# Optimization experiments

Measured on AMD Instinct MI355X. Metric: run time of the kernel, lower is better.

The kernel has to match this reference:

```python
import math
import jax, jax.numpy as jnp
import numpy as np

NH = 16          # num attention heads
NOPE = 128       # qk_nope_head_dim
ROPE = 64        # qk_rope_head_dim
VD = 128         # v_head_dim
QLR = 1536       # q_lora_rank
IH = 8           # index_n_heads
ID = 128         # index_head_dim
TOPK = 8         # index_topk
EPS = 1e-5


def layernorm(x, w, b):
    mu = jnp.mean(x, axis=-1, keepdims=True)
    var = jnp.mean((x - mu) ** 2, axis=-1, keepdims=True)
    return (x - mu) * jax.lax.rsqrt(var + EPS) * w + b


def rope_tables(dim, end, base=10000.0):
    freqs = 1.0 / (base ** (jnp.arange(0, dim, 2, dtype=jnp.float32) / dim))  # [dim//2]
    t = jnp.arange(end, dtype=jnp.float32)
    f = jnp.outer(t, freqs)  # [end, dim//2]
    return jnp.cos(f), jnp.sin(f)


def apply_rope(x, cos, sin):
    # x: [b, h, s, d]; cos/sin: [s, d//2] (interleaved real/imag pairs)
    xr, xi = x[..., 0::2], x[..., 1::2]
    c = cos[None, None, :, :]
    s = sin[None, None, :, :]
    or_, oi = xr * c - xi * s, xr * s + xi * c
    return jnp.stack([or_, oi], axis=-1).reshape(x.shape)


def setup_inputs() -> dict:
    key = jax.random.key(0)
    ks = jax.random.split(key, 16)
    H = 2048
    B, S = 2, 2048
    w = lambda k, shp: (jax.random.normal(k, shp, dtype=jnp.float32) * 0.02)
    return {
        "x": jax.random.normal(ks[0], (B, S, H), dtype=jnp.float32),
        "W_cq": w(ks[1], (H, QLR)),
        "q_norm_w": jnp.ones((QLR,), jnp.float32),
        "q_norm_b": jnp.zeros((QLR,), jnp.float32),
        "W_q": w(ks[2], (QLR, NH * (NOPE + ROPE))),
        "W_ckv": w(ks[3], (H, NH * (NOPE + ROPE))),
        "kv_norm_w": jnp.ones((NOPE,), jnp.float32),
        "kv_norm_b": jnp.zeros((NOPE,), jnp.float32),
        "W_kv": w(ks[4], (NOPE, NOPE + VD)),
        "W_o": w(ks[5], (NH * VD, H)),
        "W_ip": w(ks[6], (H, IH * ID)),
        "W_ig": w(ks[7], (H, IH)),
        "W_sq": w(ks[8], (ID, ID)),
        "W_sk": w(ks[9], (ID, ID)),
        "W_sv": w(ks[10], (ID, ID)),
        "W_io": w(ks[11], (ID, H)),
    }


def _forward(x, W_cq, q_norm_w, q_norm_b, W_q, W_ckv, kv_norm_w, kv_norm_b,
             W_kv, W_o, W_ip, W_ig, W_sq, W_sk, W_sv, W_io):
    B, S, H = x.shape
    # --- MLA dense path ---
    qc = layernorm(x @ W_cq, q_norm_w, q_norm_b)                  # [B,S,QLR]
    qp = (qc @ W_q).reshape(B, S, NH, NOPE + ROPE).transpose(0, 2, 1, 3)
    q_nope, q_pe = qp[..., :NOPE], qp[..., NOPE:]
    kvc = (x @ W_ckv).reshape(B, S, NH, ROPE + NOPE).transpose(0, 2, 1, 3)
    k_pe, kv_nope = kvc[..., :ROPE], kvc[..., ROPE:]
    kv_n = layernorm(kv_nope, kv_norm_w, kv_norm_b)               # [B,NH,S,NOPE]
    kvp = kv_n @ W_kv                                             # [B,NH,S,NOPE+VD]
    k_nope, v = kvp[..., :NOPE], kvp[..., NOPE:]
    cos, sin = rope_tables(ROPE, S)
    q_pe = apply_rope(q_pe, cos, sin)
    k_pe = apply_rope(k_pe, cos, sin)
    q = jnp.concatenate([q_nope, q_pe], axis=-1)                  # [B,NH,S,192]
    k = jnp.concatenate([k_nope, k_pe], axis=-1)
    scale = 1.0 / math.sqrt(NOPE + ROPE)
    scores = jnp.einsum("bhqd,bhkd->bhqk", q, k) * scale
    causal = jnp.triu(jnp.ones((S, S), dtype=bool), k=1)
    scores = jnp.where(causal[None, None], -jnp.inf, scores)
    probs = jax.nn.softmax(scores.astype(jnp.float32), axis=-1).astype(q.dtype)
    attn = jnp.einsum("bhqk,bhkd->bhqd", probs, v)                # [B,NH,S,VD]
    # --- NSA sparse path (lightning indexer) ---
    ist = (x @ W_ip).reshape(B, S, IH, ID).transpose(0, 2, 1, 3)  # [B,IH,S,ID]
    gate = (x @ W_ig).transpose(0, 2, 1)                          # [B,IH,S]
    _, top_idx = jax.lax.top_k(gate, TOPK)                        # [B,IH,TOPK]
    sel = jnp.take_along_axis(ist, top_idx[..., None], axis=2)    # [B,IH,TOPK,ID]
    sq, sk, sv = sel @ W_sq, sel @ W_sk, sel @ W_sv
    ss = jnp.einsum("bhqd,bhkd->bhqk", sq, sk) / math.sqrt(ID)    # [B,IH,TOPK,TOPK]
    sp = jax.nn.softmax(ss.astype(jnp.float32), axis=-1).astype(sq.dtype)
    so = jnp.einsum("bhqk,bhkd->bhqd", sp, sv)                    # [B,IH,TOPK,ID]
    sparse_out = so @ W_io                                        # [B,IH,TOPK,H]
    io = sparse_out.mean(axis=2)[:, :, None, :VD]                 # [B,IH,1,VD]
    io = jnp.broadcast_to(io, (B, IH, S, VD))
    io = jnp.repeat(io, NH // IH, axis=1)                         # [B,NH,S,VD]
    attn = attn + io
    out = attn.transpose(0, 2, 1, 3).reshape(B, S, NH * VD) @ W_o
    return out


def reference(x, W_cq, q_norm_w, q_norm_b, W_q, W_ckv, kv_norm_w, kv_norm_b,
              W_kv, W_o, W_ip, W_ig, W_sq, W_sk, W_sv, W_io):
    return _forward(x, W_cq, q_norm_w, q_norm_b, W_q, W_ckv, kv_norm_w,
                    kv_norm_b, W_kv, W_o, W_ip, W_ig, W_sq, W_sk, W_sv, W_io)
```

## Files before the change

### kernel.cpp

```cpp
#include <hip/hip_runtime.h>
#include <hip/hip_bf16.h>
#include <math.h>

#define NH    16
#define NOPE  128
#define ROPED 64
#define VD    128
#define QLR   1536
#define IH    8
#define ID    128
#define TOPK  8
#define EPSF  1e-5f
#define B_    2
#define S_    2048
#define H_    2048

using bf16 = __hip_bfloat16;
typedef __attribute__((ext_vector_type(8))) short short8;
typedef __attribute__((ext_vector_type(4))) short short4v;
typedef __attribute__((ext_vector_type(4))) float f32x4;

#define GLOBAL_AS __attribute__((address_space(1)))
#define LDS_AS    __attribute__((address_space(3)))

__device__ __forceinline__ float b2f(bf16 v) { return __bfloat162float(v); }
__device__ __forceinline__ bf16 f2b(float v) { return __float2bfloat16(v); }
__device__ __forceinline__ void stoC(float* p, float v) { *p = v; }
__device__ __forceinline__ void stoC(bf16* p, float v) { *p = __float2bfloat16(v); }

__global__ __launch_bounds__(256) void gate_k(const float* __restrict__ x,
                                              const float* __restrict__ Wg,
                                              float* __restrict__ gate) {
    const int t = threadIdx.x;
    const int wid = t >> 6, lane = t & 63;
    const int row = blockIdx.x * 4 + wid;
    const float* xp = x + (size_t)row * H_;

    float acc[8] = {};
    for (int k0 = 0; k0 < H_; k0 += 256) {
        const int kb = k0 + lane * 4;
        const f32x4 xv = *(const f32x4*)(xp + kb);
        const f32x4 w0 = *(const f32x4*)(Wg + (size_t)kb * 8);
        const f32x4 w1 = *(const f32x4*)(Wg + (size_t)kb * 8 + 4);
        const f32x4 w2 = *(const f32x4*)(Wg + (size_t)(kb + 1) * 8);
        const f32x4 w3 = *(const f32x4*)(Wg + (size_t)(kb + 1) * 8 + 4);
        const f32x4 w4 = *(const f32x4*)(Wg + (size_t)(kb + 2) * 8);
        const f32x4 w5 = *(const f32x4*)(Wg + (size_t)(kb + 2) * 8 + 4);
        const f32x4 w6 = *(const f32x4*)(Wg + (size_t)(kb + 3) * 8);
        const f32x4 w7 = *(const f32x4*)(Wg + (size_t)(kb + 3) * 8 + 4);
#pragma unroll
        for (int j = 0; j < 4; j++) {
            acc[j]     += xv[0] * w0[j] + xv[1] * w2[j] + xv[2] * w4[j] + xv[3] * w6[j];
            acc[4 + j] += xv[0] * w1[j] + xv[1] * w3[j] + xv[2] * w5[j] + xv[3] * w7[j];
        }
    }
#pragma unroll
    for (int j = 0; j < 8; j++) {
#pragma unroll
        for (int off = 32; off > 0; off >>= 1)
            acc[j] += __shfl_xor(acc[j], off);
    }
    if (lane == 0) {
#pragma unroll
        for (int j = 0; j < 8; j++) gate[(size_t)row * 8 + j] = acc[j];
    }
}

template <typename OT>
__global__ __launch_bounds__(256) void gemm_bt_mfma_k(const bf16* __restrict__ A,
                                                      const bf16* __restrict__ Bt,
                                                      OT* __restrict__ C,
                                                      int M, int N, int K) {
    __shared__ bf16 As[128 * 32];
    __shared__ bf16 Bs[128 * 32];
    const int t = threadIdx.x;
    const int w = t >> 6;
    const int l = t & 63;
    const int col = l & 15;
    const int quad = l >> 4;
    const int wm = w >> 1, wn = w & 1;

    const int gx = gridDim.x;
    const int nwg = gx * gridDim.y;
    const int lin = blockIdx.y * gx + blockIdx.x;
    const int work = (lin & 7) * (nwg >> 3) + (lin >> 3);
    const int row0 = (work / gx) * 128;
    const int col0 = (work % gx) * 128;

    const int rA = l >> 2;
    const int cA = (l & 3) * 8;
    const bf16* ga0 = A + (size_t)(row0 + w * 16 + rA) * K + cA;
    const bf16* ga1 = A + (size_t)(row0 + (4 + w) * 16 + rA) * K + cA;
    const bf16* gb0 = Bt + (size_t)(col0 + w * 16 + rA) * K + cA;
    const bf16* gb1 = Bt + (size_t)(col0 + (4 + w) * 16 + rA) * K + cA;
    bf16* lA0 = &As[w * 512];
    bf16* lA1 = &As[(4 + w) * 512];
    bf16* lB0 = &Bs[w * 512];
    bf16* lB1 = &Bs[(4 + w) * 512];

    f32x4 acc[4][4];
#pragma unroll
    for (int i = 0; i < 4; i++)
#pragma unroll
        for (int j = 0; j < 4; j++) acc[i][j] = (f32x4){0.f, 0.f, 0.f, 0.f};

    for (int k0 = 0; k0 < K; k0 += 32) {
        __syncthreads();
        __builtin_amdgcn_global_load_lds((const GLOBAL_AS void*)(ga0 + k0),
                                         (LDS_AS void*)lA0, 16, 0, 0);
        __builtin_amdgcn_global_load_lds((const GLOBAL_AS void*)(ga1 + k0),
                                         (LDS_AS void*)lA1, 16, 0, 0);
        __builtin_amdgcn_global_load_lds((const GLOBAL_AS void*)(gb0 + k0),
                                         (LDS_AS void*)lB0, 16, 0, 0);
        __builtin_amdgcn_global_load_lds((const GLOBAL_AS void*)(gb1 + k0),
                                         (LDS_AS void*)lB1, 16, 0, 0);
        __syncthreads();

        short8 af[4], bfr[4];
#pragma unroll
        for (int i = 0; i < 4; i++) {
            af[i]  = *(const short8*)&As[(wm * 64 + i * 16 + col) * 32 + quad * 8];
            bfr[i] = *(const short8*)&Bs[(wn * 64 + i * 16 + col) * 32 + quad * 8];
        }
#pragma unroll
        for (int i = 0; i < 4; i++)
#pragma unroll
            for (int j = 0; j < 4; j++)
                acc[i][j] = __builtin_amdgcn_mfma_f32_16x16x32_bf16(af[i], bfr[j], acc[i][j], 0, 0, 0);
    }

#pragma unroll
    for (int i = 0; i < 4; i++)
#pragma unroll
        for (int j = 0; j < 4; j++)
#pragma unroll
            for (int r = 0; r < 4; r++) {
                const int gr = row0 + wm * 64 + i * 16 + quad * 4 + r;
                const int gc = col0 + wn * 64 + j * 16 + col;
                stoC(C + (size_t)gr * N + gc, acc[i][j][r]);
            }
}

__global__ __launch_bounds__(256) void gemm_x3_k(const bf16* __restrict__ A,
                                                 const bf16* __restrict__ Bt,
                                                 float* __restrict__ cq,
                                                 bf16* __restrict__ kvc,
                                                 float* __restrict__ ist) {
    __shared__ bf16 As[128 * 32];
    __shared__ bf16 Bs[128 * 32];
    const int K = H_;
    const int t = threadIdx.x;
    const int w = t >> 6;
    const int l = t & 63;
    const int col = l & 15;
    const int quad = l >> 4;
    const int wm = w >> 1, wn = w & 1;

    const int gx = gridDim.x;
    const int nwg = gx * gridDim.y;
    const int lin = blockIdx.y * gx + blockIdx.x;
    const int work = (lin & 7) * (nwg >> 3) + (lin >> 3);
    const int row0 = (work / gx) * 128;
    const int col0 = (work % gx) * 128;

    const int rA = l >> 2;
    const int cA = (l & 3) * 8;
    const bf16* ga0 = A + (size_t)(row0 + w * 16 + rA) * K + cA;
    const bf16* ga1 = A + (size_t)(row0 + (4 + w) * 16 + rA) * K + cA;
    const bf16* gb0 = Bt + (size_t)(col0 + w * 16 + rA) * K + cA;
    const bf16* gb1 = Bt + (size_t)(col0 + (4 + w) * 16 + rA) * K + cA;
    bf16* lA0 = &As[w * 512];
    bf16* lA1 = &As[(4 + w) * 512];
    bf16* lB0 = &Bs[w * 512];
    bf16* lB1 = &Bs[(4 + w) * 512];

    f32x4 acc[4][4];
#pragma unroll
    for (int i = 0; i < 4; i++)
#pragma unroll
        for (int j = 0; j < 4; j++) acc[i][j] = (f32x4){0.f, 0.f, 0.f, 0.f};

    for (int k0 = 0; k0 < K; k0 += 32) {
        __syncthreads();
        __builtin_amdgcn_global_load_lds((const GLOBAL_AS void*)(ga0 + k0),
                                         (LDS_AS void*)lA0, 16, 0, 0);
        __builtin_amdgcn_global_load_lds((const GLOBAL_AS void*)(ga1 + k0),
                                         (LDS_AS void*)lA1, 16, 0, 0);
        __builtin_amdgcn_global_load_lds((const GLOBAL_AS void*)(gb0 + k0),
                                         (LDS_AS void*)lB0, 16, 0, 0);
        __builtin_amdgcn_global_load_lds((const GLOBAL_AS void*)(gb1 + k0),
                                         (LDS_AS void*)lB1, 16, 0, 0);
        __syncthreads();

        short8 af[4], bfr[4];
#pragma unroll
        for (int i = 0; i < 4; i++) {
            af[i]  = *(const short8*)&As[(wm * 64 + i * 16 + col) * 32 + quad * 8];
            bfr[i] = *(const short8*)&Bs[(wn * 64 + i * 16 + col) * 32 + quad * 8];
        }
#pragma unroll
        for (int i = 0; i < 4; i++)
#pragma unroll
            for (int j = 0; j < 4; j++)
                acc[i][j] = __builtin_amdgcn_mfma_f32_16x16x32_bf16(af[i], bfr[j], acc[i][j], 0, 0, 0);
    }

#pragma unroll
    for (int i = 0; i < 4; i++)
#pragma unroll
        for (int j = 0; j < 4; j++)
#pragma unroll
            for (int r = 0; r < 4; r++) {
                const int gr = row0 + wm * 64 + i * 16 + quad * 4 + r;
                const int gc = col0 + wn * 64 + j * 16 + col;
                const float v = acc[i][j][r];
                if (col0 < 1536)       cq[(size_t)gr * QLR + gc] = v;
                else if (col0 < 4608)  kvc[(size_t)gr * 3072 + (gc - 1536)] = f2b(v);
                else                   ist[(size_t)gr * 1024 + (gc - 4608)] = v;
            }
}

__global__ __launch_bounds__(256) void gemm_kv_k(const bf16* __restrict__ A,
                                                 const bf16* __restrict__ Bt,
                                                 bf16* __restrict__ kvc,
                                                 bf16* __restrict__ VbT) {
    __shared__ bf16 As[128 * 32];
    __shared__ bf16 Bs[128 * 32];
    const int K = 128;
    const int t = threadIdx.x;
    const int w = t >> 6;
    const int l = t & 63;
    const int col = l & 15;
    const int quad = l >> 4;
    const int wm = w >> 1, wn = w & 1;

    const int gx = gridDim.x;
    const int nwg = gx * gridDim.y;
    const int lin = blockIdx.y * gx + blockIdx.x;
    const int work = (lin & 7) * (nwg >> 3) + (lin >> 3);
    const int row0 = (work / gx) * 128;
    const int col0 = (work % gx) * 128;

    const int rA = l >> 2;
    const int cA = (l & 3) * 8;
    const bf16* ga0 = A + (size_t)(row0 + w * 16 + rA) * K + cA;
    const bf16* ga1 = A + (size_t)(row0 + (4 + w) * 16 + rA) * K + cA;
    const bf16* gb0 = Bt + (size_t)(col0 + w * 16 + rA) * K + cA;
    const bf16* gb1 = Bt + (size_t)(col0 + (4 + w) * 16 + rA) * K + cA;
    bf16* lA0 = &As[w * 512];
    bf16* lA1 = &As[(4 + w) * 512];
    bf16* lB0 = &Bs[w * 512];
    bf16* lB1 = &Bs[(4 + w) * 512];

    f32x4 acc[4][4];
#pragma unroll
    for (int i = 0; i < 4; i++)
#pragma unroll
        for (int j = 0; j < 4; j++) acc[i][j] = (f32x4){0.f, 0.f, 0.f, 0.f};

    for (int k0 = 0; k0 < K; k0 += 32) {
        __syncthreads();
        __builtin_amdgcn_global_load_lds((const GLOBAL_AS void*)(ga0 + k0),
                                         (LDS_AS void*)lA0, 16, 0, 0);
        __builtin_amdgcn_global_load_lds((const GLOBAL_AS void*)(ga1 + k0),
                                         (LDS_AS void*)lA1, 16, 0, 0);
        __builtin_amdgcn_global_load_lds((const GLOBAL_AS void*)(gb0 + k0),
                                         (LDS_AS void*)lB0, 16, 0, 0);
        __builtin_amdgcn_global_load_lds((const GLOBAL_AS void*)(gb1 + k0),
                                         (LDS_AS void*)lB1, 16, 0, 0);
        __syncthreads();

        short8 af[4], bfr[4];
#pragma unroll
        for (int i = 0; i < 4; i++) {
            af[i]  = *(const short8*)&As[(wm * 64 + i * 16 + col) * 32 + quad * 8];
            bfr[i] = *(const short8*)&Bs[(wn * 64 + i * 16 + col) * 32 + quad * 8];
        }
#pragma unroll
        for (int i = 0; i < 4; i++)
#pragma unroll
            for (int j = 0; j < 4; j++)
                acc[i][j] = __builtin_amdgcn_mfma_f32_16x16x32_bf16(af[i], bfr[j], acc[i][j], 0, 0, 0);
    }

    if (col0 == 0) {
#pragma unroll
        for (int i = 0; i < 4; i++)
#pragma unroll
            for (int j = 0; j < 4; j++)
#pragma unroll
                for (int r = 0; r < 4; r++) {
                    const int gr = row0 + wm * 64 + i * 16 + quad * 4 + r;
                    const int gc = wn * 64 + j * 16 + col;
                    kvc[(size_t)gr * 192 + gc] = f2b(acc[i][j][r]);
                }
    } else {
        const int bb = row0 >> 15;
        const int ssb = ((row0 >> 4) & (S_ - 1)) + wm * 4;
#pragma unroll
        for (int j = 0; j < 4; j++) {
            const int dv = wn * 64 + j * 16 + col;
#pragma unroll
            for (int r = 0; r < 4; r++) {
                const int hh = quad * 4 + r;
                short4v pk;
#pragma unroll
                for (int i = 0; i < 4; i++) {
                    bf16 v = f2b(acc[i][j][r]);
                    pk[i] = *(short*)&v;
                }
                *(short4v*)&VbT[((size_t)(bb * NH + hh) * 128 + dv) * S_ + ssb] = pk;
            }
        }
    }
}

__global__ __launch_bounds__(256) void kv_ln_k(bf16* __restrict__ kvc,
                                               const float* __restrict__ knw,
                                               const float* __restrict__ knb,
                                               bf16* __restrict__ kvn) {
    const int idx = blockIdx.x * 4 + (threadIdx.x >> 6);
    const int lane = threadIdx.x & 63;
    const int s = (idx >> 4) & (S_ - 1);
    const size_t base = (size_t)idx * 192;

    const float v0 = b2f(kvc[base + 64 + lane]);
    const float v1 = b2f(kvc[base + 128 + lane]);
    float xr = 0.f, xi = 0.f;
    if (lane < 32) { xr = b2f(kvc[base + 2 * lane]); xi = b2f(kvc[base + 2 * lane + 1]); }

    float s1 = v0 + v1, s2 = v0 * v0 + v1 * v1;
#pragma unroll
    for (int off = 32; off > 0; off >>= 1) {
        s1 += __shfl_xor(s1, off);
        s2 += __shfl_xor(s2, off);
    }
    const float mu = s1 * (1.f / 128.f);
    const float rinv = rsqrtf(s2 * (1.f / 128.f) - mu * mu + EPSF);
    kvn[(size_t)idx * 128 + lane]      = f2b((v0 - mu) * rinv * knw[lane] + knb[lane]);
    kvn[(size_t)idx * 128 + lane + 64] = f2b((v1 - mu) * rinv * knw[lane + 64] + knb[lane + 64]);

    if (lane < 32) {
        const float freq = exp2f(-0.41524101186092014f * (float)lane);
        const float ang = (float)s * freq;
        float sn, c; sincosf(ang, &sn, &c);
        kvc[base + 128 + 2 * lane]     = f2b(xr * c - xi * sn);
        kvc[base + 128 + 2 * lane + 1] = f2b(xr * sn + xi * c);
    }
}

__global__ __launch_bounds__(256) void cast_bf16_k(const float* __restrict__ X,
                                                   bf16* __restrict__ Y, int n4) {
    for (int i = blockIdx.x * 256 + threadIdx.x; i < n4; i += gridDim.x * 256) {
        const f32x4 v = ((const f32x4*)X)[i];
        short4v o;
#pragma unroll
        for (int j = 0; j < 4; j++) {
            bf16 b = f2b(v[j]);
            o[j] = *(short*)&b;
        }
        ((short4v*)Y)[i] = o;
    }
}

__global__ __launch_bounds__(256) void transpose_cast_k(const float* __restrict__ W,
                                                        bf16* __restrict__ Wt,
                                                        int K, int N) {
    __shared__ float tile[32][33];
    const int t = threadIdx.x;
    const int tx = t & 31, ty = t >> 5;
    const int n0 = blockIdx.x * 32;
    const int k0 = blockIdx.y * 32;
#pragma unroll
    for (int i = 0; i < 4; i++)
        tile[ty + 8 * i][tx] = W[(size_t)(k0 + ty + 8 * i) * N + n0 + tx];
    __syncthreads();
#pragma unroll
    for (int i = 0; i < 4; i++)
        Wt[(size_t)(n0 + ty + 8 * i) * K + k0 + tx] = f2b(tile[tx][ty + 8 * i]);
}

__global__ __launch_bounds__(256) void layernorm_cast_k(const float* __restrict__ X,
                                                        const float* __restrict__ w,
                                                        const float* __restrict__ b,
                                                        bf16* __restrict__ Y,
                                                        int L) {
    __shared__ float r1[256], r2[256];
    const int row = blockIdx.x;
    const int t = threadIdx.x;
    const float* xp = X + (size_t)row * L;
    bf16* yp = Y + (size_t)row * L;
    float s1 = 0.f, s2 = 0.f;
    for (int j = t; j < L; j += 256) { const float v = xp[j]; s1 += v; s2 += v * v; }
    r1[t] = s1; r2[t] = s2; __syncthreads();
    for (int off = 128; off > 0; off >>= 1) {
        if (t < off) { r1[t] += r1[t + off]; r2[t] += r2[t + off]; }
        __syncthreads();
    }
    const float mu   = r1[0] / (float)L;
    const float var  = r2[0] / (float)L - mu * mu;
    const float rinv = rsqrtf(var + EPSF);
    for (int j = t; j < L; j += 256)
        yp[j] = f2b((xp[j] - mu) * rinv * w[j] + b[j]);
}

__global__ __launch_bounds__(256) void q_rope_k(bf16* __restrict__ qp) {
    const int total = B_ * S_ * NH * 32;
    for (int p = blockIdx.x * 256 + threadIdx.x; p < total; p += gridDim.x * 256) {
        const int j = p & 31;
        const int row = p >> 5;
        const int sr = row >> 4;
        const int s = sr & (S_ - 1);
        const size_t base = (size_t)row * 192 + 128 + 2 * j;
        const float xr = b2f(qp[base]);
        const float xi = b2f(qp[base + 1]);
        const float freq = exp2f(-0.41524101186092014f * (float)j);
        const float ang = (float)s * freq;
        float sn, c; sincosf(ang, &sn, &c);
        qp[base]     = f2b(xr * c - xi * sn);
        qp[base + 1] = f2b(xr * sn + xi * c);
    }
}

__global__ __launch_bounds__(256) void sparse_k(const float* __restrict__ gate,
                                                const float* __restrict__ ist,
                                                const float* __restrict__ Wsq,
                                                const float* __restrict__ Wsk,
                                                const float* __restrict__ Wsv,
                                                const float* __restrict__ Wio,
                                                float* __restrict__ io) {
    __shared__ float g[S_];
    __shared__ float sel[TOPK][ID];
    __shared__ float sq[TOPK][ID], sk[TOPK][ID], sv[TOPK][ID];
    __shared__ float sp[TOPK][TOPK];
    __shared__ float ms[ID];
    __shared__ float rv[256];
    __shared__ int ri[256];
    __shared__ int sidx[TOPK];
    const int bi = blockIdx.x;
    const int ih = bi % IH;
    const int b = bi / IH;
    const int t = threadIdx.x;

    for (int s = t; s < S_; s += 256) g[s] = gate[(size_t)(b * S_ + s) * IH + ih];
    __syncthreads();

    for (int r = 0; r < TOPK; r++) {
        float bv = -INFINITY; int bx = S_;
        for (int s = t; s < S_; s += 256) {
            const float v = g[s];
            if (v > bv) { bv = v; bx = s; }
        }
        rv[t] = bv; ri[t] = bx; __syncthreads();
        for (int off = 128; off > 0; off >>= 1) {
            if (t < off) {
                const float v2 = rv[t + off]; const int i2 = ri[t + off];
                if (v2 > rv[t] || (v2 == rv[t] && i2 < ri[t])) { rv[t] = v2; ri[t] = i2; }
            }
            __syncthreads();
        }
        if (t == 0) { sidx[r] = ri[0]; g[ri[0]] = -INFINITY; }
        __syncthreads();
    }

    for (int i = t; i < TOPK * ID; i += 256) {
        const int r = i >> 7, d = i & 127;
        sel[r][d] = ist[((size_t)(b * S_ + sidx[r]) * IH + ih) * ID + d];
    }
    __syncthreads();

    for (int i = t; i < TOPK * ID; i += 256) {
        const int r = i >> 7, n = i & 127;
        float aq = 0.f, ak = 0.f, av = 0.f;
        for (int k = 0; k < 128; k++) {
            const float s = sel[r][k];
            aq += s * Wsq[k * ID + n];
            ak += s * Wsk[k * ID + n];
            av += s * Wsv[k * ID + n];
        }
        sq[r][n] = aq; sk[r][n] = ak; sv[r][n] = av;
    }
    __syncthreads();

    if (t < TOPK * TOPK) {
        const int r = t >> 3, c = t & 7;
        float a = 0.f;
        for (int k = 0; k < 128; k++) a += sq[r][k] * sk[c][k];
        sp[r][c] = a * 0.08838834764831845f;
    }
    __syncthreads();

    if (t < TOPK) {
        float m = -INFINITY;
        for (int c = 0; c < 8; c++) m = fmaxf(m, sp[t][c]);
        float e[8]; float sum = 0.f;
        for (int c = 0; c < 8; c++) { e[c] = expf(sp[t][c] - m); sum += e[c]; }
        for (int c = 0; c < 8; c++) sp[t][c] = e[c] / sum;
    }
    __syncthreads();

    if (t < ID) {
        float acc = 0.f;
        for (int r = 0; r < 8; r++) {
            float so = 0.f;
            for (int c = 0; c < 8; c++) so += sp[r][c] * sv[c][t];
            acc += so;
        }
        ms[t] = acc * 0.125f;
    }
    __syncthreads();

    if (t < ID) {
        float acc = 0.f;
        for (int k = 0; k < 128; k++) acc += ms[k] * Wio[(size_t)k * H_ + t];
        io[((size_t)b * IH + ih) * ID + t] = acc;
    }
}

__global__ __launch_bounds__(256, 2) void attn_mfma_k(const bf16* __restrict__ Qp,
                                                      const bf16* __restrict__ Kc,
                                                      const bf16* __restrict__ VbT,
                                                      const float* __restrict__ io,
                                                      bf16* __restrict__ O) {
    __shared__ unsigned short Kt[64 * 200];
    __shared__ unsigned short Vt[128 * 72];
    __shared__ unsigned short Ps[4 * 16 * 72];

    const int lin = blockIdx.x;
    const int qt = 31 - (lin >> 5);
    const int hb = lin & 31;
    const int h = hb & 15;
    const int b = hb >> 4;
    const int q0 = qt * 64;

    const int t = threadIdx.x;
    const int lane = t & 63;
    const int wq = t >> 6;
    const int col = lane & 15;
    const int quad = lane >> 4;

    const float scale = 0.07216878364870322f;
    const bf16* vplane = VbT + (size_t)(b * NH + h) * 128 * (size_t)S_;

    const int kr = t >> 2;
    const int kc0 = (t & 3) * 48;
    const int vki0 = (t & 7) * 8;
    const int vdv = t >> 3;

    short8 qfrag[6];
    {
        const int q = q0 + wq * 16 + col;
        const short8* qrow = (const short8*)(Qp + ((size_t)(b * S_ + q) * NH + h) * 192);
#pragma unroll
        for (int kc = 0; kc < 6; kc++) qfrag[kc] = qrow[kc * 4 + quad];
    }

    float m_r[4], l_r[4];
#pragma unroll
    for (int r = 0; r < 4; r++) { m_r[r] = -1e30f; l_r[r] = 0.f; }
    f32x4 accO[8];
#pragma unroll
    for (int nt = 0; nt < 8; nt++) accO[nt] = (f32x4){0.f, 0.f, 0.f, 0.f};

    const int nkt = qt + 1;

    short8 kreg[6], vreg[4];
    {
        const short8* ksrc = (const short8*)(Kc + ((size_t)(b * S_ + kr) * NH + h) * 192 + kc0);
#pragma unroll
        for (int c = 0; c < 6; c++) kreg[c] = ksrc[c];
#pragma unroll
        for (int p = 0; p < 4; p++)
            vreg[p] = *(const short8*)(vplane + (size_t)(p * 32 + vdv) * S_ + vki0);
    }

    for (int kt = 0; kt < nkt; kt++) {
        const int kt0 = kt * 64;
        __syncthreads();
        {
            short8* dst = (short8*)&Kt[kr * 200 + kc0];
#pragma unroll
            for (int c = 0; c < 6; c++) dst[c] = kreg[c];
#pragma unroll
            for (int p = 0; p < 4; p++)
                *(short8*)&Vt[(p * 32 + vdv) * 72 + vki0] = vreg[p];
        }
        __syncthreads();

        if (kt + 1 < nkt) {
            const int nk0 = kt0 + 64;
            const short8* ksrc = (const short8*)(Kc + ((size_t)(b * S_ + nk0 + kr) * NH + h) * 192 + kc0);
#pragma unroll
            for (int c = 0; c < 6; c++) kreg[c] = ksrc[c];
#pragma unroll
            for (int p = 0; p < 4; p++)
                vreg[p] = *(const short8*)(vplane + (size_t)(p * 32 + vdv) * S_ + nk0 + vki0);
        }

        f32x4 s[4];
        __builtin_amdgcn_s_setprio(1);
#pragma unroll
        for (int nt = 0; nt < 4; nt++) {
            f32x4 acc = (f32x4){0.f, 0.f, 0.f, 0.f};
#pragma unroll
            for (int kc = 0; kc < 6; kc++) {
                const short8 kf = *(const short8*)&Kt[(nt * 16 + col) * 200 + kc * 32 + quad * 8];
                acc = __builtin_amdgcn_mfma_f32_16x16x32_bf16(qfrag[kc], kf, acc, 0, 0, 0);
            }
            s[nt] = acc;
        }
        __builtin_amdgcn_s_setprio(0);
#pragma unroll
        for (int nt = 0; nt < 4; nt++)
#pragma unroll
            for (int r = 0; r < 4; r++) {
                const int kg = kt0 + nt * 16 + col;
                const int qg = q0 + wq * 16 + quad * 4 + r;
                const float v = s[nt][r] * scale;
                s[nt][r] = (kg > qg) ? -1e30f : v;
            }
        float alpha[4];
#pragma unroll
        for (int r = 0; r < 4; r++) {
            float mt = fmaxf(fmaxf(s[0][r], s[1][r]), fmaxf(s[2][r], s[3][r]));
            mt = fmaxf(mt, __shfl_xor(mt, 1));
            mt = fmaxf(mt, __shfl_xor(mt, 2));
            mt = fmaxf(mt, __shfl_xor(mt, 4));
            mt = fmaxf(mt, __shfl_xor(mt, 8));
            const bool need = (mt > m_r[r] + 8.f);
            const float mn = need ? mt : m_r[r];
            alpha[r] = need ? __expf(m_r[r] - mn) : 1.f;
            m_r[r] = mn;
            float rs = 0.f;
#pragma unroll
            for (int nt = 0; nt < 4; nt++) {
                const float p = __expf(s[nt][r] - mn);
                s[nt][r] = p;
                rs += p;
            }
            rs += __shfl_xor(rs, 1);
            rs += __shfl_xor(rs, 2);
            rs += __shfl_xor(rs, 4);
            rs += __shfl_xor(rs, 8);
            l_r[r] = l_r[r] * alpha[r] + rs;
        }
        {
            unsigned short* pw = &Ps[wq * 1152];
#pragma unroll
            for (int nt = 0; nt < 4; nt++)
#pragma unroll
                for (int r = 0; r < 4; r++) {
                    bf16 hv = f2b(s[nt][r]);
                    pw[(quad * 4 + r) * 72 + nt * 16 + col] = *(unsigned short*)&hv;
                }
        }
        short8 pf[2];
#pragma unroll
        for (int kk = 0; kk < 2; kk++)
            pf[kk] = *(const short8*)&Ps[wq * 1152 + col * 72 + kk * 32 + quad * 8];
        if (!(alpha[0] == 1.f && alpha[1] == 1.f && alpha[2] == 1.f && alpha[3] == 1.f)) {
#pragma unroll
            for (int nt = 0; nt < 8; nt++)
#pragma unroll
                for (int r = 0; r < 4; r++) accO[nt][r] *= alpha[r];
        }
        __builtin_amdgcn_s_setprio(1);
#pragma unroll
        for (int nt = 0; nt < 8; nt++) {
#pragma unroll
            for (int kk = 0; kk < 2; kk++) {
                const short8 vf = *(const short8*)&Vt[(nt * 16 + col) * 72 + kk * 32 + quad * 8];
                accO[nt] = __builtin_amdgcn_mfma_f32_16x16x32_bf16(pf[kk], vf, accO[nt], 0, 0, 0);
            }
        }
        __builtin_amdgcn_s_setprio(0);
    }

    const float* iorow = io + ((size_t)b * IH + (h >> 1)) * ID;
    float rinv[4];
#pragma unroll
    for (int r = 0; r < 4; r++) rinv[r] = 1.f / l_r[r];
#pragma unroll
    for (int nt = 0; nt < 8; nt++) {
        const int dv = nt * 16 + col;
        const float iov = iorow[dv];
#pragma unroll
        for (int r = 0; r < 4; r++) {
            const int q = q0 + wq * 16 + quad * 4 + r;
            O[((size_t)(b * S_ + q) * NH + h) * VD + dv] = f2b(accO[nt][r] * rinv[r] + iov);
        }
    }
}

extern "C" void kernel_launch(void* const* d_in, const int* in_sizes, int n_in,
                              void* d_out, int out_size, void* d_ws, size_t ws_size,
                              hipStream_t stream) {
    const float* x      = (const float*)d_in[0];
    const float* W_cq   = (const float*)d_in[1];
    const float* qn_w   = (const float*)d_in[2];
    const float* qn_b   = (const float*)d_in[3];
    const float* W_q    = (const float*)d_in[4];
    const float* W_ckv  = (const float*)d_in[5];
    const float* kvn_w  = (const float*)d_in[6];
    const float* kvn_b  = (const float*)d_in[7];
    const float* W_kv   = (const float*)d_in[8];
    const float* W_o    = (const float*)d_in[9];
    const float* W_ip   = (const float*)d_in[10];
    const float* W_ig   = (const float*)d_in[11];
    const float* W_sq   = (const float*)d_in[12];
    const float* W_sk   = (const float*)d_in[13];
    const float* W_sv   = (const float*)d_in[14];
    const float* W_io   = (const float*)d_in[15];
    float* out = (float*)d_out;

    const int M = B_ * S_;

    char* wsb = (char*)d_ws;
    bf16*  WtM   = (bf16*)wsb;
    bf16*  cqb   = (bf16*)wsb;
    bf16*  WqT   = (bf16*)(wsb + 12582912);
    bf16*  kvn   = (bf16*)wsb;
    bf16*  attnb = (bf16*)wsb;
    bf16*  WoT   = (bf16*)(wsb + 16777216);
    float* cq    = (float*)(wsb + 33554432);
    bf16*  qp    = (bf16*)(wsb + 33554432);
    bf16*  kvc   = (bf16*)(wsb + 58720256);
    float* ist   = (float*)(wsb + 83886080);
    bf16*  VbT   = (bf16*)(wsb + 83886080);
    float* gate  = (float*)(wsb + 100663296);
    bf16*  WkvT  = (bf16*)(wsb + 100663296);
    float* iob   = (float*)(wsb + 100794368);
    bf16*  xb    = (bf16*)d_out;

    dim3 blk(256);

    cast_bf16_k<<<dim3(2048), blk, 0, stream>>>(x, xb, M * H_ / 4);

    transpose_cast_k<<<dim3(QLR / 32, H_ / 32), blk, 0, stream>>>(W_cq, WtM, H_, QLR);
    transpose_cast_k<<<dim3(3072 / 32, H_ / 32), blk, 0, stream>>>(W_ckv, WtM + (size_t)1536 * H_, H_, 3072);
    transpose_cast_k<<<dim3(1024 / 32, H_ / 32), blk, 0, stream>>>(W_ip, WtM + (size_t)4608 * H_, H_, 1024);

    gemm_x3_k<<<dim3(5632 / 128, M / 128), blk, 0, stream>>>(xb, WtM, cq, kvc, ist);

    layernorm_cast_k<<<dim3(M), blk, 0, stream>>>(cq, qn_w, qn_b, cqb, QLR);

    transpose_cast_k<<<dim3(3072 / 32, QLR / 32), blk, 0, stream>>>(W_q, WqT, QLR, 3072);
    gemm_bt_mfma_k<bf16><<<dim3(3072 / 128, M / 128), blk, 0, stream>>>(cqb, WqT, qp, M, 3072, QLR);

    gate_k<<<dim3(M / 4), blk, 0, stream>>>(x, W_ig, gate);

    q_rope_k<<<dim3(2048), blk, 0, stream>>>(qp);

    kv_ln_k<<<dim3(B_ * S_ * NH / 4), blk, 0, stream>>>(kvc, kvn_w, kvn_b, kvn);

    sparse_k<<<dim3(B_ * IH), blk, 0, stream>>>(gate, ist, W_sq, W_sk, W_sv, W_io, iob);

    transpose_cast_k<<<dim3(256 / 32, 128 / 32), blk, 0, stream>>>(W_kv, WkvT, 128, 256);
    gemm_kv_k<<<dim3(2, (B_ * S_ * NH) / 128), blk, 0, stream>>>(kvn, WkvT, kvc, VbT);

    attn_mfma_k<<<dim3(1024), blk, 0, stream>>>(qp, kvc, VbT, iob, attnb);

    transpose_cast_k<<<dim3(H_ / 32, H_ / 32), blk, 0, stream>>>(W_o, WoT, H_, H_);
    gemm_bt_mfma_k<float><<<dim3(H_ / 128, M / 128), blk, 0, stream>>>(attnb, WoT, out, M, H_, H_);
}
```

Baseline: 678.9 us.

## Compute index projection only for top-k rows and fuse q RoPE into GEMM

Drops the full W_ip projection from the fused x GEMM, which removes one weight transpose and about a fifth of that GEMM's columns. The sparse kernel now computes the index projection only for the TOPK selected rows, straight from fp32 x and W_ip. The q RoPE rotation moves into the q GEMM epilogue using lane shuffles, so the separate rope kernel pass over qp goes away. The risk is that the 16 sparse blocks each now do serial fp32 GEMV work over 2048x128 of weights per selected row, which could lengthen that kernel.

```diff
diff --git a/kernel.cpp b/kernel.cpp
--- a/kernel.cpp
+++ b/kernel.cpp
@@ -141,11 +141,10 @@
             }
 }
 
-__global__ __launch_bounds__(256) void gemm_x3_k(const bf16* __restrict__ A,
+__global__ __launch_bounds__(256) void gemm_x2_k(const bf16* __restrict__ A,
                                                  const bf16* __restrict__ Bt,
                                                  float* __restrict__ cq,
-                                                 bf16* __restrict__ kvc,
-                                                 float* __restrict__ ist) {
+                                                 bf16* __restrict__ kvc) {
     __shared__ bf16 As[128 * 32];
     __shared__ bf16 Bs[128 * 32];
     const int K = H_;
@@ -214,10 +213,102 @@
                 const int gr = row0 + wm * 64 + i * 16 + quad * 4 + r;
                 const int gc = col0 + wn * 64 + j * 16 + col;
                 const float v = acc[i][j][r];
-                if (col0 < 1536)       cq[(size_t)gr * QLR + gc] = v;
-                else if (col0 < 4608)  kvc[(size_t)gr * 3072 + (gc - 1536)] = f2b(v);
-                else                   ist[(size_t)gr * 1024 + (gc - 4608)] = v;
-            }
+                if (col0 < 1536) cq[(size_t)gr * QLR + gc] = v;
+                else             kvc[(size_t)gr * 3072 + (gc - 1536)] = f2b(v);
+            }
+}
+
+__global__ __launch_bounds__(256) void gemm_q_rope_k(const bf16* __restrict__ A,
+                                                     const bf16* __restrict__ Bt,
+                                                     bf16* __restrict__ qp) {
+    __shared__ bf16 As[128 * 32];
+    __shared__ bf16 Bs[128 * 32];
+    const int K = QLR;
+    const int N = 3072;
+    const int t = threadIdx.x;
+    const int w = t >> 6;
+    const int l = t & 63;
+    const int col = l & 15;
+    const int quad = l >> 4;
+    const int wm = w >> 1, wn = w & 1;
+
+    const int gx = gridDim.x;
+    const int nwg = gx * gridDim.y;
+    const int lin = blockIdx.y * gx + blockIdx.x;
+    const int work = (lin & 7) * (nwg >> 3) + (lin >> 3);
+    const int row0 = (work / gx) * 128;
+    const int col0 = (work % gx) * 128;
+
+    const int rA = l >> 2;
+    const int cA = (l & 3) * 8;
+    const bf16* ga0 = A + (size_t)(row0 + w * 16 + rA) * K + cA;
+    const bf16* ga1 = A + (size_t)(row0 + (4 + w) * 16 + rA) * K + cA;
+    const bf16* gb0 = Bt + (size_t)(col0 + w * 16 + rA) * K + cA;
+    const bf16* gb1 = Bt + (size_t)(col0 + (4 + w) * 16 + rA) * K + cA;
+    bf16* lA0 = &As[w * 512];
+    bf16* lA1 = &As[(4 + w) * 512];
+    bf16* lB0 = &Bs[w * 512];
+    bf16* lB1 = &Bs[(4 + w) * 512];
+
+    f32x4 acc[4][4];
+#pragma unroll
+    for (int i = 0; i < 4; i++)
+#pragma unroll
+        for (int j = 0; j < 4; j++) acc[i][j] = (f32x4){0.f, 0.f, 0.f, 0.f};
+
+    for (int k0 = 0; k0 < K; k0 += 32) {
+        __syncthreads();
+        __builtin_amdgcn_global_load_lds((const GLOBAL_AS void*)(ga0 + k0),
+                                         (LDS_AS void*)lA0, 16, 0, 0);
+        __builtin_amdgcn_global_load_lds((const GLOBAL_AS void*)(ga1 + k0),
+                                         (LDS_AS void*)lA1, 16, 0, 0);
+        __builtin_amdgcn_global_load_lds((const GLOBAL_AS void*)(gb0 + k0),
+                                         (LDS_AS void*)lB0, 16, 0, 0);
+        __builtin_amdgcn_global_load_lds((const GLOBAL_AS void*)(gb1 + k0),
+                                         (LDS_AS void*)lB1, 16, 0, 0);
+        __syncthreads();
+
+        short8 af[4], bfr[4];
+#pragma unroll
+        for (int i = 0; i < 4; i++) {
+            af[i]  = *(const short8*)&As[(wm * 64 + i * 16 + col) * 32 + quad * 8];
+            bfr[i] = *(const short8*)&Bs[(wn * 64 + i * 16 + col) * 32 + quad * 8];
+        }
+#pragma unroll
+        for (int i = 0; i < 4; i++)
+#pragma unroll
+            for (int j = 0; j < 4; j++)
+                acc[i][j] = __builtin_amdgcn_mfma_f32_16x16x32_bf16(af[i], bfr[j], acc[i][j], 0, 0, 0);
+    }
+
+#pragma unroll
+    for (int i = 0; i < 4; i++)
+#pragma unroll
+        for (int j = 0; j < 4; j++) {
+            const int g0 = col0 + wn * 64 + j * 16;
+            const int c0 = g0 % 192;
+            if (c0 >= 128) {
+                const int jj = ((c0 - 128) >> 1) + (col >> 1);
+                const float freq = exp2f(-0.41524101186092014f * (float)jj);
+#pragma unroll
+                for (int r = 0; r < 4; r++) {
+                    const int gr = row0 + wm * 64 + i * 16 + quad * 4 + r;
+                    const int s = gr & (S_ - 1);
+                    const float own = acc[i][j][r];
+                    const float other = __shfl_xor(own, 1);
+                    float sn, cs; sincosf((float)s * freq, &sn, &cs);
+                    const float v = (col & 1) ? (other * sn + own * cs)
+                                              : (own * cs - other * sn);
+                    qp[(size_t)gr * N + g0 + col] = f2b(v);
+                }
+            } else {
+#pragma unroll
+                for (int r = 0; r < 4; r++) {
+                    const int gr = row0 + wm * 64 + i * 16 + quad * 4 + r;
+                    qp[(size_t)gr * N + g0 + col] = f2b(acc[i][j][r]);
+                }
+            }
+        }
 }
 
 __global__ __launch_bounds__(256) void gemm_kv_k(const bf16* __restrict__ A,
@@ -404,26 +495,9 @@
         yp[j] = f2b((xp[j] - mu) * rinv * w[j] + b[j]);
 }
 
-__global__ __launch_bounds__(256) void q_rope_k(bf16* __restrict__ qp) {
-    const int total = B_ * S_ * NH * 32;
-    for (int p = blockIdx.x * 256 + threadIdx.x; p < total; p += gridDim.x * 256) {
-        const int j = p & 31;
-        const int row = p >> 5;
-        const int sr = row >> 4;
-        const int s = sr & (S_ - 1);
-        const size_t base = (size_t)row * 192 + 128 + 2 * j;
-        const float xr = b2f(qp[base]);
-        const float xi = b2f(qp[base + 1]);
-        const float freq = exp2f(-0.41524101186092014f * (float)j);
-        const float ang = (float)s * freq;
-        float sn, c; sincosf(ang, &sn, &c);
-        qp[base]     = f2b(xr * c - xi * sn);
-        qp[base + 1] = f2b(xr * sn + xi * c);
-    }
-}
-
 __global__ __launch_bounds__(256) void sparse_k(const float* __restrict__ gate,
-                                                const float* __restrict__ ist,
+                                                const float* __restrict__ x,
+                                                const float* __restrict__ Wip,
                                                 const float* __restrict__ Wsq,
                                                 const float* __restrict__ Wsk,
                                                 const float* __restrict__ Wsv,
@@ -463,9 +537,31 @@
         __syncthreads();
     }
 
-    for (int i = t; i < TOPK * ID; i += 256) {
-        const int r = i >> 7, d = i & 127;
-        sel[r][d] = ist[((size_t)(b * S_ + sidx[r]) * IH + ih) * ID + d];
+    {
+        float* sc = &sq[0][0];
+        const int n4 = (t & 31) * 4;
+        const int kc = (t >> 5) * 256;
+        for (int r = 0; r < TOPK; r++) {
+            const float* xrow = x + ((size_t)b * S_ + sidx[r]) * H_;
+            __syncthreads();
+            for (int k = t; k < H_; k += 256) g[k] = xrow[k];
+            __syncthreads();
+            f32x4 a4 = (f32x4){0.f, 0.f, 0.f, 0.f};
+            for (int k = 0; k < 256; k++) {
+                const float xv = g[kc + k];
+                const f32x4 wv = *(const f32x4*)&Wip[(size_t)(kc + k) * (IH * ID) + ih * ID + n4];
+#pragma unroll
+                for (int e = 0; e < 4; e++) a4[e] += xv * wv[e];
+            }
+            *(f32x4*)&sc[(t >> 5) * 128 + n4] = a4;
+            __syncthreads();
+            if (t < ID) {
+                float a = 0.f;
+#pragma unroll
+                for (int c = 0; c < 8; c++) a += sc[c * 128 + t];
+                sel[r][t] = a;
+            }
+        }
     }
     __syncthreads();
 
@@ -725,7 +821,6 @@
     float* cq    = (float*)(wsb + 33554432);
     bf16*  qp    = (bf16*)(wsb + 33554432);
     bf16*  kvc   = (bf16*)(wsb + 58720256);
-    float* ist   = (float*)(wsb + 83886080);
     bf16*  VbT   = (bf16*)(wsb + 83886080);
     float* gate  = (float*)(wsb + 100663296);
     bf16*  WkvT  = (bf16*)(wsb + 100663296);
@@ -738,22 +833,19 @@
 
     transpose_cast_k<<<dim3(QLR / 32, H_ / 32), blk, 0, stream>>>(W_cq, WtM, H_, QLR);
     transpose_cast_k<<<dim3(3072 / 32, H_ / 32), blk, 0, stream>>>(W_ckv, WtM + (size_t)1536 * H_, H_, 3072);
-    transpose_cast_k<<<dim3(1024 / 32, H_ / 32), blk, 0, stream>>>(W_ip, WtM + (size_t)4608 * H_, H_, 1024);
-
-    gemm_x3_k<<<dim3(5632 / 128, M / 128), blk, 0, stream>>>(xb, WtM, cq, kvc, ist);
+
+    gemm_x2_k<<<dim3(4608 / 128, M / 128), blk, 0, stream>>>(xb, WtM, cq, kvc);
 
     layernorm_cast_k<<<dim3(M), blk, 0, stream>>>(cq, qn_w, qn_b, cqb, QLR);
 
     transpose_cast_k<<<dim3(3072 / 32, QLR / 32), blk, 0, stream>>>(W_q, WqT, QLR, 3072);
-    gemm_bt_mfma_k<bf16><<<dim3(3072 / 128, M / 128), blk, 0, stream>>>(cqb, WqT, qp, M, 3072, QLR);
+    gemm_q_rope_k<<<dim3(3072 / 128, M / 128), blk, 0, stream>>>(cqb, WqT, qp);
 
     gate_k<<<dim3(M / 4), blk, 0, stream>>>(x, W_ig, gate);
 
-    q_rope_k<<<dim3(2048), blk, 0, stream>>>(qp);
-
     kv_ln_k<<<dim3(B_ * S_ * NH / 4), blk, 0, stream>>>(kvc, kvn_w, kvn_b, kvn);
 
-    sparse_k<<<dim3(B_ * IH), blk, 0, stream>>>(gate, ist, W_sq, W_sk, W_sv, W_io, iob);
+    sparse_k<<<dim3(B_ * IH), blk, 0, stream>>>(gate, x, W_ip, W_sq, W_sk, W_sv, W_io, iob);
 
     transpose_cast_k<<<dim3(256 / 32, 128 / 32), blk, 0, stream>>>(W_kv, WkvT, 128, 256);
     gemm_kv_k<<<dim3(2, (B_ * S_ * NH) / 128), blk, 0, stream>>>(kvn, WkvT, kvc, VbT);
```

After: 786.3 us. 15.8% more time.

## Compute indexer projection only for top-k selected rows instead of all tokens

Applied to the files above, without the earlier changes.

Drops the W_ip columns from the fused input GEMM and removes the transpose of W_ip. Top-k selection now runs in its own kernel, and a new sel_k kernel projects only the 8 selected x rows per (batch, head) through W_ip in fp32, split across 8 K-chunks. sparse_k then sums those partial results. This avoids a 4096x1024x2048 GEMM slice and its output write, at the cost of two extra small launches and fp32 rather than bf16 projection numerics.

```diff
diff --git a/kernel.cpp b/kernel.cpp
--- a/kernel.cpp
+++ b/kernel.cpp
@@ -141,11 +141,10 @@
             }
 }
 
-__global__ __launch_bounds__(256) void gemm_x3_k(const bf16* __restrict__ A,
+__global__ __launch_bounds__(256) void gemm_x2_k(const bf16* __restrict__ A,
                                                  const bf16* __restrict__ Bt,
                                                  float* __restrict__ cq,
-                                                 bf16* __restrict__ kvc,
-                                                 float* __restrict__ ist) {
+                                                 bf16* __restrict__ kvc) {
     __shared__ bf16 As[128 * 32];
     __shared__ bf16 Bs[128 * 32];
     const int K = H_;
@@ -214,9 +213,8 @@
                 const int gr = row0 + wm * 64 + i * 16 + quad * 4 + r;
                 const int gc = col0 + wn * 64 + j * 16 + col;
                 const float v = acc[i][j][r];
-                if (col0 < 1536)       cq[(size_t)gr * QLR + gc] = v;
-                else if (col0 < 4608)  kvc[(size_t)gr * 3072 + (gc - 1536)] = f2b(v);
-                else                   ist[(size_t)gr * 1024 + (gc - 4608)] = v;
+                if (col0 < 1536) cq[(size_t)gr * QLR + gc] = v;
+                else             kvc[(size_t)gr * 3072 + (gc - 1536)] = f2b(v);
             }
 }
 
@@ -422,21 +420,11 @@
     }
 }
 
-__global__ __launch_bounds__(256) void sparse_k(const float* __restrict__ gate,
-                                                const float* __restrict__ ist,
-                                                const float* __restrict__ Wsq,
-                                                const float* __restrict__ Wsk,
-                                                const float* __restrict__ Wsv,
-                                                const float* __restrict__ Wio,
-                                                float* __restrict__ io) {
+__global__ __launch_bounds__(256) void topk_k(const float* __restrict__ gate,
+                                              int* __restrict__ sidx_buf) {
     __shared__ float g[S_];
-    __shared__ float sel[TOPK][ID];
-    __shared__ float sq[TOPK][ID], sk[TOPK][ID], sv[TOPK][ID];
-    __shared__ float sp[TOPK][TOPK];
-    __shared__ float ms[ID];
     __shared__ float rv[256];
     __shared__ int ri[256];
-    __shared__ int sidx[TOPK];
     const int bi = blockIdx.x;
     const int ih = bi % IH;
     const int b = bi / IH;
@@ -459,13 +447,81 @@
             }
             __syncthreads();
         }
-        if (t == 0) { sidx[r] = ri[0]; g[ri[0]] = -INFINITY; }
-        __syncthreads();
-    }
+        if (t == 0) { sidx_buf[bi * TOPK + r] = ri[0]; g[ri[0]] = -INFINITY; }
+        __syncthreads();
+    }
+}
+
+__global__ __launch_bounds__(256) void sel_k(const int* __restrict__ sidx_buf,
+                                             const float* __restrict__ x,
+                                             const float* __restrict__ Wip,
+                                             float* __restrict__ sel_part) {
+    __shared__ float xs[TOPK][256];
+    __shared__ float sc[8 * 128];
+    const int kc = blockIdx.x;
+    const int bi = blockIdx.y;
+    const int ih = bi % IH;
+    const int b = bi / IH;
+    const int t = threadIdx.x;
+
+    for (int i = t; i < TOPK * 256; i += 256) {
+        const int r = i >> 8, k = i & 255;
+        const int row = sidx_buf[bi * TOPK + r];
+        xs[r][k] = x[((size_t)(b * S_ + row)) * H_ + kc * 256 + k];
+    }
+    __syncthreads();
+
+    const int n4 = (t & 31) * 4;
+    const int kg = t >> 5;
+    f32x4 aa[8];
+#pragma unroll
+    for (int r = 0; r < 8; r++) aa[r] = (f32x4){0.f, 0.f, 0.f, 0.f};
+    for (int k = 0; k < 32; k++) {
+        const int kk = kg * 32 + k;
+        const f32x4 wv = *(const f32x4*)&Wip[(size_t)(kc * 256 + kk) * (IH * ID) + ih * ID + n4];
+#pragma unroll
+        for (int r = 0; r < 8; r++) {
+            const float xv = xs[r][kk];
+#pragma unroll
+            for (int e = 0; e < 4; e++) aa[r][e] += xv * wv[e];
+        }
+    }
+#pragma unroll
+    for (int r = 0; r < 8; r++) {
+        *(f32x4*)&sc[kg * 128 + n4] = aa[r];
+        __syncthreads();
+        if (t < ID) {
+            float a = 0.f;
+#pragma unroll
+            for (int c = 0; c < 8; c++) a += sc[c * 128 + t];
+            sel_part[(((size_t)kc * 16 + bi) * TOPK + r) * ID + t] = a;
+        }
+        __syncthreads();
+    }
+}
+
+__global__ __launch_bounds__(256) void sparse_k(const float* __restrict__ sel_part,
+                                                const float* __restrict__ Wsq,
+                                                const float* __restrict__ Wsk,
+                                                const float* __restrict__ Wsv,
+                                                const float* __restrict__ Wio,
+                                                float* __restrict__ io) {
+    __shared__ float sel[TOPK][ID];
+    __shared__ float sq[TOPK][ID], sk[TOPK][ID], sv[TOPK][ID];
+    __shared__ float sp[TOPK][TOPK];
+    __shared__ float ms[ID];
+    const int bi = blockIdx.x;
+    const int ih = bi % IH;
+    const int b = bi / IH;
+    const int t = threadIdx.x;
 
     for (int i = t; i < TOPK * ID; i += 256) {
-        const int r = i >> 7, d = i & 127;
-        sel[r][d] = ist[((size_t)(b * S_ + sidx[r]) * IH + ih) * ID + d];
+        const int r = i >> 7, n = i & 127;
+        float a = 0.f;
+#pragma unroll
+        for (int c = 0; c < 8; c++)
+            a += sel_part[(((size_t)c * 16 + bi) * TOPK + r) * ID + n];
+        sel[r][n] = a;
     }
     __syncthreads();
 
@@ -725,7 +781,8 @@
     float* cq    = (float*)(wsb + 33554432);
     bf16*  qp    = (bf16*)(wsb + 33554432);
     bf16*  kvc   = (bf16*)(wsb + 58720256);
-    float* ist   = (float*)(wsb + 83886080);
+    float* selp  = (float*)(wsb + 83886080);
+    int*   sidxb = (int*)(wsb + 83886080 + 524288);
     bf16*  VbT   = (bf16*)(wsb + 83886080);
     float* gate  = (float*)(wsb + 100663296);
     bf16*  WkvT  = (bf16*)(wsb + 100663296);
@@ -738,22 +795,23 @@
 
     transpose_cast_k<<<dim3(QLR / 32, H_ / 32), blk, 0, stream>>>(W_cq, WtM, H_, QLR);
     transpose_cast_k<<<dim3(3072 / 32, H_ / 32), blk, 0, stream>>>(W_ckv, WtM + (size_t)1536 * H_, H_, 3072);
-    transpose_cast_k<<<dim3(1024 / 32, H_ / 32), blk, 0, stream>>>(W_ip, WtM + (size_t)4608 * H_, H_, 1024);
-
-    gemm_x3_k<<<dim3(5632 / 128, M / 128), blk, 0, stream>>>(xb, WtM, cq, kvc, ist);
+
+    gemm_x2_k<<<dim3(4608 / 128, M / 128), blk, 0, stream>>>(xb, WtM, cq, kvc);
 
     layernorm_cast_k<<<dim3(M), blk, 0, stream>>>(cq, qn_w, qn_b, cqb, QLR);
 
     transpose_cast_k<<<dim3(3072 / 32, QLR / 32), blk, 0, stream>>>(W_q, WqT, QLR, 3072);
     gemm_bt_mfma_k<bf16><<<dim3(3072 / 128, M / 128), blk, 0, stream>>>(cqb, WqT, qp, M, 3072, QLR);
+    q_rope_k<<<dim3(2048), blk, 0, stream>>>(qp);
 
     gate_k<<<dim3(M / 4), blk, 0, stream>>>(x, W_ig, gate);
 
-    q_rope_k<<<dim3(2048), blk, 0, stream>>>(qp);
+    topk_k<<<dim3(B_ * IH), blk, 0, stream>>>(gate, sidxb);
+    sel_k<<<dim3(8, B_ * IH), blk, 0, stream>>>(sidxb, x, W_ip, selp);
 
     kv_ln_k<<<dim3(B_ * S_ * NH / 4), blk, 0, stream>>>(kvc, kvn_w, kvn_b, kvn);
 
-    sparse_k<<<dim3(B_ * IH), blk, 0, stream>>>(gate, ist, W_sq, W_sk, W_sv, W_io, iob);
+    sparse_k<<<dim3(B_ * IH), blk, 0, stream>>>(selp, W_sq, W_sk, W_sv, W_io, iob);
 
     transpose_cast_k<<<dim3(256 / 32, 128 / 32), blk, 0, stream>>>(W_kv, WkvT, 128, 256);
     gemm_kv_k<<<dim3(2, (B_ * S_ * NH) / 128), blk, 0, stream>>>(kvn, WkvT, kvc, VbT);
```

Measured after the change: 675.5 us. About the same (-0.5%).
